# Kernel tuning notes

Measured on AMD Instinct MI355X. Metric: run time of the kernel, lower is better.

Reference implementation:

```python
import jax, jax.numpy as jnp
import numpy as np


def setup_inputs() -> dict:
    key = jax.random.key(0)
    B, D, KD, TR, NI = 4096, 512, 448, 64, 16  # batch, d_model, key_dim_size, t_resolution, num_iters
    DK = KD + TR                                # full query/key width = 512
    ks = jax.random.split(key, 9)

    def w(k, fan_in, fan_out):
        return jax.random.normal(k, (fan_in, fan_out), jnp.float32) / jnp.sqrt(jnp.float32(fan_in))

    return {
        "x":   jax.random.normal(ks[0], (B, D), jnp.float32),
        "Wik": w(ks[1], D, KD),        # input_key_proj
        "Wiv": w(ks[2], D, D),         # input_value_proj (value dim = d_model)
        "Wq":  w(ks[3], D, DK),        # query_proj
        "Wk":  w(ks[4], D + TR, DK),   # key_proj on concat(block_out, sin(t*t_enc))
        "Wv":  w(ks[5], D, D),         # value_proj
        "W1":  w(ks[6], D, D),         # block MLP layer 1
        "W2":  w(ks[7], D, D),         # block MLP layer 2
        "t_emb": 0.02 * jax.random.normal(ks[8], (NI + 1, D), jnp.float32),  # block time conditioning
    }


def reference(x, Wik, Wiv, Wq, Wk, Wv, W1, W2, t_emb):
    B, D = x.shape
    DK = Wq.shape[1]
    TR = Wk.shape[0] - D           # t_resolution
    NI = t_emb.shape[0] - 1        # num_iters
    dt = x.dtype
    scale = jnp.asarray(1.0 / np.sqrt(DK), dt)
    # t_encoding = pi * (1/2)**i
    t_enc = jnp.pi * (0.5 ** jnp.arange(TR, dtype=dt))

    def attend(q, K, V, n):  # q:[B,DK], K:[B,NI,DK], V:[B,NI,D]; n static valid length
        s = jnp.einsum('bd,btd->bt', q, K[:, :n]) * scale
        p = jax.nn.softmax(s, axis=-1)
        return jnp.einsum('bt,btd->bd', p, V[:, :n])

    def block(A, t):  # opaque self.block(A, t=t): MLP with per-t conditioning
        return jax.nn.gelu(A @ W1 + t_emb[t]) @ W2

    # preallocated growing KV cache (in-place append instead of concat)
    K = jnp.zeros((B, NI, DK), dt)
    V = jnp.zeros((B, NI, D), dt)
    k0 = jnp.pad(x @ Wik, ((0, 0), (0, TR)))  # initial key padded to DK (sin(0)=0 encoding)
    K = K.at[:, 0].set(k0)
    V = V.at[:, 0].set(x @ Wiv)
    q = jnp.ones((B, DK), dt)

    for t in range(NI - 1):  # static unrolled recurrence over iterations
        A = attend(q, K, V, t + 1)
        Bt = block(A, t)
        sin_t = jnp.broadcast_to(jnp.sin(t * t_enc), (B, TR))
        K = K.at[:, t + 1].set(jnp.concatenate([Bt, sin_t], axis=-1) @ Wk)
        V = V.at[:, t + 1].set(Bt @ Wv)
        q = Bt @ Wq

    A = attend(q, K, V, NI)
    return block(A, NI)  # final block call with t = num_iters
```

## Files before the change

### kernel.cpp

```cpp
#include <hip/hip_runtime.h>
#include <hip/hip_bf16.h>
#include <math.h>

typedef unsigned short u16;
using bf16x8 = __attribute__((ext_vector_type(8))) short;
using f32x4  = __attribute__((ext_vector_type(4))) float;

__device__ inline float b2f(u16 u) {
  unsigned v = ((unsigned)u) << 16;
  return __builtin_bit_cast(float, v);
}
__device__ inline u16 f2b(float f) {
  unsigned u = __builtin_bit_cast(unsigned, f);
  u += 0x7fffu + ((u >> 16) & 1u);
  return (u16)(u >> 16);
}
__device__ inline float gelu_f(float x) {
  float x3 = x * x * x;
  return 0.5f * x * (1.f + tanhf(0.7978845608028654f * (x + 0.044715f * x3)));
}
__device__ inline void gload_lds16(const void* g, void* lds) {
  __builtin_amdgcn_global_load_lds((const __attribute__((address_space(1))) void*)g,
                                   (__attribute__((address_space(3))) void*)lds,
                                   16, 0, 0);
}

#define EPI_SPLIT2 0
#define EPI_F32    1

template<int EPI>
__global__ __launch_bounds__(256)
void gemm64(const u16* __restrict__ Aptr, int lda,
            const u16* __restrict__ BT,
            void* __restrict__ out0, void* __restrict__ out1,
            const u16* __restrict__ fvec, int t1)
{
  constexpr int BM = 128, BN = 64, WN = 32, NR = 2, MR = 4;
  __shared__ alignas(16) char Ash[2][BM * 128];
  __shared__ alignas(16) char Bsh[2][BN * 128];
  const int tid = threadIdx.x, lane = tid & 63, wid = tid >> 6;
  const int wm = wid >> 1, wn = wid & 1;
  const int bm = blockIdx.x, bn = blockIdx.y;

  const int rIn = lane >> 3;
  const int c16log = (lane & 7) ^ (rIn & 7);

  auto stage = [&](int buf, int kt) {
    #pragma unroll
    for (int i = 0; i < 4; ++i) {
      int c = wid * 4 + i;
      int row = c * 8 + rIn;
      gload_lds16(Aptr + (size_t)(bm * BM + row) * lda + kt + c16log * 8,
                  Ash[buf] + c * 1024);
    }
    #pragma unroll
    for (int i = 0; i < 2; ++i) {
      int c = wid * 2 + i;
      int row = c * 8 + rIn;
      gload_lds16(BT + (size_t)(bn * BN + row) * 512 + kt + c16log * 8,
                  Bsh[buf] + c * 1024);
    }
  };

  f32x4 acc[MR][NR] = {};
  stage(0, 0);
  #pragma unroll
  for (int kt = 0; kt < 8; ++kt) {
    const int c = kt & 1;
    if (kt < 7) stage(c ^ 1, (kt + 1) * 64);
    if (kt < 7) asm volatile("s_waitcnt vmcnt(6)" ::: "memory");
    else        asm volatile("s_waitcnt vmcnt(0)" ::: "memory");
    __builtin_amdgcn_s_barrier();
    asm volatile("" ::: "memory");
    #pragma unroll
    for (int kk = 0; kk < 64; kk += 32) {
      bf16x8 af[MR], bfr[NR];
      #pragma unroll
      for (int m = 0; m < MR; ++m) {
        int R = wm * 64 + m * 16 + (lane & 15);
        int c16 = (kk >> 3) + (lane >> 4);
        af[m] = *(const bf16x8*)(Ash[c] + R * 128 + ((c16 ^ (R & 7)) << 4));
      }
      #pragma unroll
      for (int n = 0; n < NR; ++n) {
        int R = wn * WN + n * 16 + (lane & 15);
        int c16 = (kk >> 3) + (lane >> 4);
        bfr[n] = *(const bf16x8*)(Bsh[c] + R * 128 + ((c16 ^ (R & 7)) << 4));
      }
      #pragma unroll
      for (int m = 0; m < MR; ++m)
        #pragma unroll
        for (int n = 0; n < NR; ++n)
          acc[m][n] = __builtin_amdgcn_mfma_f32_16x16x32_bf16(af[m], bfr[n], acc[m][n], 0, 0, 0);
    }
    asm volatile("" ::: "memory");
    __builtin_amdgcn_s_barrier();
    asm volatile("" ::: "memory");
  }

  const int row0 = bm * BM + wm * 64;
  const int col0 = bn * BN + wn * WN;
  #pragma unroll
  for (int m = 0; m < MR; ++m) {
    #pragma unroll
    for (int n = 0; n < NR; ++n) {
      #pragma unroll
      for (int i = 0; i < 4; ++i) {
        int row = row0 + m * 16 + (lane >> 4) * 4 + i;
        int col = col0 + n * 16 + (lane & 15);
        float v = acc[m][n][i];
        if constexpr (EPI == EPI_SPLIT2) {
          if (col < 512) {
            ((u16*)out0)[((size_t)row * 16 + t1) * 512 + col] = f2b(v + b2f(fvec[col]));
          } else {
            ((u16*)out1)[((size_t)row * 16 + t1) * 512 + (col - 512)] = f2b(v);
          }
        } else {
          ((float*)out0)[(size_t)row * 512 + col] = v;
        }
      }
    }
  }
}

struct BatchJobs {
  const u16* A[5];
  const u16* BT[5];
  u16* O[5];
  int M[5];
};

__global__ __launch_bounds__(256)
void gemm_batch(BatchJobs jb)
{
  constexpr int BM = 128, BN = 64, WN = 32, NR = 2, MR = 4;
  const int z = blockIdx.z;
  if ((int)blockIdx.x * BM >= jb.M[z]) return;
  const u16* __restrict__ Aptr = jb.A[z];
  const u16* __restrict__ BT   = jb.BT[z];
  u16* __restrict__ Optr       = jb.O[z];

  __shared__ alignas(16) char Ash[2][BM * 128];
  __shared__ alignas(16) char Bsh[2][BN * 128];
  const int tid = threadIdx.x, lane = tid & 63, wid = tid >> 6;
  const int wm = wid >> 1, wn = wid & 1;
  const int bm = blockIdx.x, bn = blockIdx.y;

  const int rIn = lane >> 3;
  const int c16log = (lane & 7) ^ (rIn & 7);

  auto stage = [&](int buf, int kt) {
    #pragma unroll
    for (int i = 0; i < 4; ++i) {
      int c = wid * 4 + i;
      int row = c * 8 + rIn;
      gload_lds16(Aptr + (size_t)(bm * BM + row) * 512 + kt + c16log * 8,
                  Ash[buf] + c * 1024);
    }
    #pragma unroll
    for (int i = 0; i < 2; ++i) {
      int c = wid * 2 + i;
      int row = c * 8 + rIn;
      gload_lds16(BT + (size_t)(bn * BN + row) * 512 + kt + c16log * 8,
                  Bsh[buf] + c * 1024);
    }
  };

  f32x4 acc[MR][NR] = {};
  stage(0, 0);
  #pragma unroll
  for (int kt = 0; kt < 8; ++kt) {
    const int c = kt & 1;
    if (kt < 7) stage(c ^ 1, (kt + 1) * 64);
    if (kt < 7) asm volatile("s_waitcnt vmcnt(6)" ::: "memory");
    else        asm volatile("s_waitcnt vmcnt(0)" ::: "memory");
    __builtin_amdgcn_s_barrier();
    asm volatile("" ::: "memory");
    #pragma unroll
    for (int kk = 0; kk < 64; kk += 32) {
      bf16x8 af[MR], bfr[NR];
      #pragma unroll
      for (int m = 0; m < MR; ++m) {
        int R = wm * 64 + m * 16 + (lane & 15);
        int c16 = (kk >> 3) + (lane >> 4);
        af[m] = *(const bf16x8*)(Ash[c] + R * 128 + ((c16 ^ (R & 7)) << 4));
      }
      #pragma unroll
      for (int n = 0; n < NR; ++n) {
        int R = wn * WN + n * 16 + (lane & 15);
        int c16 = (kk >> 3) + (lane >> 4);
        bfr[n] = *(const bf16x8*)(Bsh[c] + R * 128 + ((c16 ^ (R & 7)) << 4));
      }
      #pragma unroll
      for (int m = 0; m < MR; ++m)
        #pragma unroll
        for (int n = 0; n < NR; ++n)
          acc[m][n] = __builtin_amdgcn_mfma_f32_16x16x32_bf16(af[m], bfr[n], acc[m][n], 0, 0, 0);
    }
    asm volatile("" ::: "memory");
    __builtin_amdgcn_s_barrier();
    asm volatile("" ::: "memory");
  }

  const int row0 = bm * BM + wm * 64;
  const int col0 = bn * BN + wn * WN;
  #pragma unroll
  for (int m = 0; m < MR; ++m)
    #pragma unroll
    for (int n = 0; n < NR; ++n)
      #pragma unroll
      for (int i = 0; i < 4; ++i) {
        int row = row0 + m * 16 + (lane >> 4) * 4 + i;
        int col = col0 + n * 16 + (lane & 15);
        Optr[(size_t)row * 512 + col] = f2b(acc[m][n][i]);
      }
}

__global__ __launch_bounds__(256)
void attend_kernel(const u16* __restrict__ qv, const u16* __restrict__ Kc,
                   const u16* __restrict__ VWc, u16* __restrict__ Hout,
                   const float* __restrict__ temb, int n)
{
  const int lane = threadIdx.x & 63;
  const int w = threadIdx.x >> 6;
  const int b = blockIdx.x * 4 + w;
  const float scale = 0.04419417382415922f;
  const size_t base = (size_t)b * 512 + lane * 8;
  bf16x8 q8 = *(const bf16x8*)(qv + base);
  float qf[8];
  #pragma unroll
  for (int j = 0; j < 8; ++j) qf[j] = b2f((u16)q8[j]);
  float s[16];
  float mx = -1e30f;
  #pragma unroll
  for (int t = 0; t < 16; ++t) {
    if (t < n) {
      bf16x8 k8 = *(const bf16x8*)(Kc + ((size_t)b * 16 + t) * 512 + lane * 8);
      float d = 0.f;
      #pragma unroll
      for (int j = 0; j < 8; ++j) d += qf[j] * b2f((u16)k8[j]);
      #pragma unroll
      for (int off = 32; off > 0; off >>= 1) d += __shfl_xor(d, off, 64);
      s[t] = d * scale;
      mx = fmaxf(mx, s[t]);
    }
  }
  float p[16], sum = 0.f;
  #pragma unroll
  for (int t = 0; t < 16; ++t) if (t < n) { p[t] = expf(s[t] - mx); sum += p[t]; }
  const float inv = 1.f / sum;
  float a[8] = {};
  #pragma unroll
  for (int t = 0; t < 16; ++t) {
    if (t < n) {
      bf16x8 v8 = *(const bf16x8*)(VWc + ((size_t)b * 16 + t) * 512 + lane * 8);
      float pt = p[t] * inv;
      #pragma unroll
      for (int j = 0; j < 8; ++j) a[j] += pt * b2f((u16)v8[j]);
    }
  }
  bf16x8 o;
  #pragma unroll
  for (int j = 0; j < 8; ++j)
    o[j] = (short)f2b(gelu_f(a[j] + temb[lane * 8 + j]));
  *(bf16x8*)(Hout + base) = o;
}

__global__ __launch_bounds__(256)
void prep_kernel(const float* __restrict__ x,   const float* __restrict__ Wik,
                 const float* __restrict__ Wiv, const float* __restrict__ Wq,
                 const float* __restrict__ Wk,  const float* __restrict__ Wv,
                 const float* __restrict__ W1,  const float* __restrict__ W2,
                 u16* __restrict__ W1T, u16* __restrict__ W2T, u16* __restrict__ WqT,
                 u16* __restrict__ WkT, u16* __restrict__ WvT,
                 u16* __restrict__ W2b, u16* __restrict__ Wivb, u16* __restrict__ xb,
                 u16* __restrict__ Wikpadb, u16* __restrict__ biasKpad)
{
  const int bid = blockIdx.x, tid = threadIdx.x;
  if (bid < 1280) {
    __shared__ float tile[32][33];
    const int mat = bid >> 8, local = bid & 255;
    const float* in = (mat == 0) ? W1 : (mat == 1) ? W2 : (mat == 2) ? Wq
                    : (mat == 3) ? Wk : Wv;
    u16* out = (mat == 0) ? W1T : (mat == 1) ? W2T : (mat == 2) ? WqT
             : (mat == 3) ? WkT : WvT;
    const int tx = tid & 31, ty = tid >> 5;
    const int c0 = (local & 15) * 32, r0 = (local >> 4) * 32;
    #pragma unroll
    for (int rr = 0; rr < 32; rr += 8)
      tile[ty + rr][tx] = in[(size_t)(r0 + ty + rr) * 512 + c0 + tx];
    __syncthreads();
    #pragma unroll
    for (int rr = 0; rr < 32; rr += 8)
      out[(size_t)(c0 + ty + rr) * 512 + r0 + tx] = f2b(tile[tx][ty + rr]);
  } else if (bid < 3840) {
    const float* in; u16* out; int local;
    if (bid < 1536)      { in = W2;  out = W2b;  local = bid - 1280; }
    else if (bid < 1792) { in = Wiv; out = Wivb; local = bid - 1536; }
    else                 { in = x;   out = xb;   local = bid - 1792; }
    const int i = local * 256 + tid;
    const float4 v = ((const float4*)in)[i];
    ushort4 o;
    o.x = f2b(v.x); o.y = f2b(v.y); o.z = f2b(v.z); o.w = f2b(v.w);
    ((ushort4*)out)[i] = o;
  } else if (bid < 4096) {
    const int local = bid - 3840;
    const int e = local * 1024 + tid * 4;
    const int r = e >> 9, c0 = e & 511;
    ushort4 o;
    float v0 = (c0 + 0 < 448) ? Wik[(size_t)r * 448 + c0 + 0] : 0.f;
    float v1 = (c0 + 1 < 448) ? Wik[(size_t)r * 448 + c0 + 1] : 0.f;
    float v2 = (c0 + 2 < 448) ? Wik[(size_t)r * 448 + c0 + 2] : 0.f;
    float v3 = (c0 + 3 < 448) ? Wik[(size_t)r * 448 + c0 + 3] : 0.f;
    o.x = f2b(v0); o.y = f2b(v1); o.z = f2b(v2); o.w = f2b(v3);
    *(ushort4*)(Wikpadb + (size_t)r * 512 + c0) = o;
  } else {
    const int local = bid - 4096;
    const int t = local >> 1;
    const int col = ((local & 1) << 8) + tid;
    float acc = 0.f;
    if (t < 15) {
      #pragma unroll
      for (int r = 0; r < 64; ++r) {
        float tenc = 3.14159265358979323846f * exp2f(-(float)r);
        acc += sinf((float)t * tenc) * Wk[(size_t)(512 + r) * 512 + col];
      }
    }
    biasKpad[(size_t)t * 512 + col] = f2b(acc);
  }
}

extern "C" void kernel_launch(void* const* d_in, const int* in_sizes, int n_in,
                              void* d_out, int out_size, void* d_ws, size_t ws_size,
                              hipStream_t stream)
{
  const float* x    = (const float*)d_in[0];
  const float* Wik  = (const float*)d_in[1];
  const float* Wiv  = (const float*)d_in[2];
  const float* Wq   = (const float*)d_in[3];
  const float* Wk   = (const float*)d_in[4];
  const float* Wv   = (const float*)d_in[5];
  const float* W1   = (const float*)d_in[6];
  const float* W2   = (const float*)d_in[7];
  const float* temb = (const float*)d_in[8];

  char* ws = (char*)d_ws;
  size_t off = 0;
  auto alloc = [&](size_t bytes) {
    char* p = ws + off;
    off += (bytes + 255) & ~(size_t)255;
    return p;
  };
  const size_t SQ = (size_t)512 * 512 * 2;
  u16* W1T     = (u16*)alloc(SQ);
  u16* W2T     = (u16*)alloc(SQ);
  u16* WqT     = (u16*)alloc(SQ);
  u16* WkT     = (u16*)alloc(SQ);
  u16* WvT     = (u16*)alloc(SQ);
  u16* W2b     = (u16*)alloc(SQ);
  u16* Wivb    = (u16*)alloc(SQ);
  u16* Wikpadb = (u16*)alloc(SQ);
  u16* biasKpad= (u16*)alloc((size_t)128 * 512 * 2);
  u16* W2Wq    = (u16*)alloc(SQ);
  u16* W2WkD   = (u16*)alloc(SQ);
  u16* W2Wv    = (u16*)alloc(SQ);
  u16* biasC   = (u16*)alloc((size_t)128 * 512 * 2);
  u16* PT2     = (u16*)alloc((size_t)1024 * 512 * 2);
  u16* ITn     = (u16*)alloc((size_t)1024 * 512 * 2);
  u16* xb      = (u16*)alloc((size_t)4096 * 512 * 2);
  u16* Kc      = (u16*)alloc((size_t)4096 * 16 * 512 * 2);
  u16* VWc     = (u16*)alloc((size_t)4096 * 16 * 512 * 2);
  u16* Hb      = (u16*)alloc((size_t)4096 * 512 * 2);

  dim3 blk(256);
  prep_kernel<<<dim3(4352), blk, 0, stream>>>(
      x, Wik, Wiv, Wq, Wk, Wv, W1, W2,
      W1T, W2T, WqT, WkT, WvT, W2b, Wivb, xb, Wikpadb, biasKpad);

  BatchJobs b1 = {};
  b1.A[0] = W2b; b1.BT[0] = WqT; b1.O[0] = W2Wq;  b1.M[0] = 512;
  b1.A[1] = W2b; b1.BT[1] = WkT; b1.O[1] = W2WkD; b1.M[1] = 512;
  b1.A[2] = W2b; b1.BT[2] = WvT; b1.O[2] = W2Wv;  b1.M[2] = 512;
  gemm_batch<<<dim3(4, 8, 3), blk, 0, stream>>>(b1);

  BatchJobs b2 = {};
  b2.A[0] = W2Wq;     b2.BT[0] = W2WkD;   b2.O[0] = PT2;                       b2.M[0] = 512;
  b2.A[1] = W1T;      b2.BT[1] = W2Wv;    b2.O[1] = PT2 + (size_t)512 * 512;   b2.M[1] = 512;
  b2.A[2] = W2Wq;     b2.BT[2] = Wikpadb; b2.O[2] = ITn;                       b2.M[2] = 512;
  b2.A[3] = W1T;      b2.BT[3] = Wivb;    b2.O[3] = ITn + (size_t)512 * 512;   b2.M[3] = 512;
  b2.A[4] = biasKpad; b2.BT[4] = W2Wq;    b2.O[4] = biasC;                     b2.M[4] = 128;
  gemm_batch<<<dim3(4, 8, 5), blk, 0, stream>>>(b2);

  gemm64<EPI_SPLIT2><<<dim3(32, 16), blk, 0, stream>>>(
      xb, 512, ITn, Kc, VWc, biasC + (size_t)15 * 512, 0);

  for (int t = 0; t < 15; ++t) {
    attend_kernel<<<dim3(1024), blk, 0, stream>>>(
        Hb, Kc, VWc, Hb, temb + (size_t)t * 512, t + 1);
    gemm64<EPI_SPLIT2><<<dim3(32, 16), blk, 0, stream>>>(
        Hb, 512, PT2, Kc, VWc, biasC + (size_t)t * 512, t + 1);
  }
  attend_kernel<<<dim3(1024), blk, 0, stream>>>(
      Hb, Kc, VWc, Hb, temb + (size_t)16 * 512, 16);
  gemm64<EPI_F32><<<dim3(32, 8), blk, 0, stream>>>(
      Hb, 512, W2T, d_out, nullptr, nullptr, 0);
}
```

Measured before the change: 519.7 us.

## Triple-buffer GEMM K-loop and fold first attend step into initial projection epilogue

The GEMM kernels move from double to triple buffering of their LDS tiles, issuing loads two k-tiles ahead with adjusted waitcnt thresholds so more memory latency is hidden. The initial projection GEMM gets a new epilogue that writes K/V slot 0 and also computes the first hidden state directly as gelu(v + temb[0]). This works because the first attention over a single key is an identity on V, so one attend launch is removed and the loop is reordered. The cost is 50% more LDS per block, which may lower occupancy, plus extra per-element GELU work in the init epilogue.

```diff
diff --git a/kernel.cpp b/kernel.cpp
--- a/kernel.cpp
+++ b/kernel.cpp
@@ -27,17 +27,18 @@
 
 #define EPI_SPLIT2 0
 #define EPI_F32    1
+#define EPI_INIT2H 2
 
 template<int EPI>
 __global__ __launch_bounds__(256)
 void gemm64(const u16* __restrict__ Aptr, int lda,
             const u16* __restrict__ BT,
-            void* __restrict__ out0, void* __restrict__ out1,
-            const u16* __restrict__ fvec, int t1)
+            void* __restrict__ out0, void* __restrict__ out1, void* __restrict__ out2,
+            const u16* __restrict__ fvec, const float* __restrict__ tembv, int t1)
 {
   constexpr int BM = 128, BN = 64, WN = 32, NR = 2, MR = 4;
-  __shared__ alignas(16) char Ash[2][BM * 128];
-  __shared__ alignas(16) char Bsh[2][BN * 128];
+  __shared__ alignas(16) char Ash[3][BM * 128];
+  __shared__ alignas(16) char Bsh[3][BN * 128];
   const int tid = threadIdx.x, lane = tid & 63, wid = tid >> 6;
   const int wm = wid >> 1, wn = wid & 1;
   const int bm = blockIdx.x, bn = blockIdx.y;
@@ -64,12 +65,18 @@
 
   f32x4 acc[MR][NR] = {};
   stage(0, 0);
+  stage(1, 64);
   #pragma unroll
   for (int kt = 0; kt < 8; ++kt) {
-    const int c = kt & 1;
-    if (kt < 7) stage(c ^ 1, (kt + 1) * 64);
-    if (kt < 7) asm volatile("s_waitcnt vmcnt(6)" ::: "memory");
-    else        asm volatile("s_waitcnt vmcnt(0)" ::: "memory");
+    const int cb = kt % 3;
+    if (kt < 6) {
+      stage((kt + 2) % 3, (kt + 2) * 64);
+      asm volatile("s_waitcnt vmcnt(12)" ::: "memory");
+    } else if (kt == 6) {
+      asm volatile("s_waitcnt vmcnt(6)" ::: "memory");
+    } else {
+      asm volatile("s_waitcnt vmcnt(0)" ::: "memory");
+    }
     __builtin_amdgcn_s_barrier();
     asm volatile("" ::: "memory");
     #pragma unroll
@@ -79,13 +86,13 @@
       for (int m = 0; m < MR; ++m) {
         int R = wm * 64 + m * 16 + (lane & 15);
         int c16 = (kk >> 3) + (lane >> 4);
-        af[m] = *(const bf16x8*)(Ash[c] + R * 128 + ((c16 ^ (R & 7)) << 4));
+        af[m] = *(const bf16x8*)(Ash[cb] + R * 128 + ((c16 ^ (R & 7)) << 4));
       }
       #pragma unroll
       for (int n = 0; n < NR; ++n) {
         int R = wn * WN + n * 16 + (lane & 15);
         int c16 = (kk >> 3) + (lane >> 4);
-        bfr[n] = *(const bf16x8*)(Bsh[c] + R * 128 + ((c16 ^ (R & 7)) << 4));
+        bfr[n] = *(const bf16x8*)(Bsh[cb] + R * 128 + ((c16 ^ (R & 7)) << 4));
       }
       #pragma unroll
       for (int m = 0; m < MR; ++m)
@@ -115,6 +122,14 @@
           } else {
             ((u16*)out1)[((size_t)row * 16 + t1) * 512 + (col - 512)] = f2b(v);
           }
+        } else if constexpr (EPI == EPI_INIT2H) {
+          if (col < 512) {
+            ((u16*)out0)[(size_t)row * 16 * 512 + col] = f2b(v);
+          } else {
+            ((u16*)out1)[(size_t)row * 16 * 512 + (col - 512)] = f2b(v);
+            ((u16*)out2)[(size_t)row * 512 + (col - 512)] =
+                f2b(gelu_f(v + tembv[col - 512]));
+          }
         } else {
           ((float*)out0)[(size_t)row * 512 + col] = v;
         }
@@ -140,8 +155,8 @@
   const u16* __restrict__ BT   = jb.BT[z];
   u16* __restrict__ Optr       = jb.O[z];
 
-  __shared__ alignas(16) char Ash[2][BM * 128];
-  __shared__ alignas(16) char Bsh[2][BN * 128];
+  __shared__ alignas(16) char Ash[3][BM * 128];
+  __shared__ alignas(16) char Bsh[3][BN * 128];
   const int tid = threadIdx.x, lane = tid & 63, wid = tid >> 6;
   const int wm = wid >> 1, wn = wid & 1;
   const int bm = blockIdx.x, bn = blockIdx.y;
@@ -168,12 +183,18 @@
 
   f32x4 acc[MR][NR] = {};
   stage(0, 0);
+  stage(1, 64);
   #pragma unroll
   for (int kt = 0; kt < 8; ++kt) {
-    const int c = kt & 1;
-    if (kt < 7) stage(c ^ 1, (kt + 1) * 64);
-    if (kt < 7) asm volatile("s_waitcnt vmcnt(6)" ::: "memory");
-    else        asm volatile("s_waitcnt vmcnt(0)" ::: "memory");
+    const int cb = kt % 3;
+    if (kt < 6) {
+      stage((kt + 2) % 3, (kt + 2) * 64);
+      asm volatile("s_waitcnt vmcnt(12)" ::: "memory");
+    } else if (kt == 6) {
+      asm volatile("s_waitcnt vmcnt(6)" ::: "memory");
+    } else {
+      asm volatile("s_waitcnt vmcnt(0)" ::: "memory");
+    }
     __builtin_amdgcn_s_barrier();
     asm volatile("" ::: "memory");
     #pragma unroll
@@ -183,13 +204,13 @@
       for (int m = 0; m < MR; ++m) {
         int R = wm * 64 + m * 16 + (lane & 15);
         int c16 = (kk >> 3) + (lane >> 4);
-        af[m] = *(const bf16x8*)(Ash[c] + R * 128 + ((c16 ^ (R & 7)) << 4));
+        af[m] = *(const bf16x8*)(Ash[cb] + R * 128 + ((c16 ^ (R & 7)) << 4));
       }
       #pragma unroll
       for (int n = 0; n < NR; ++n) {
         int R = wn * WN + n * 16 + (lane & 15);
         int c16 = (kk >> 3) + (lane >> 4);
-        bfr[n] = *(const bf16x8*)(Bsh[c] + R * 128 + ((c16 ^ (R & 7)) << 4));
+        bfr[n] = *(const bf16x8*)(Bsh[cb] + R * 128 + ((c16 ^ (R & 7)) << 4));
       }
       #pragma unroll
       for (int m = 0; m < MR; ++m)
@@ -391,17 +412,16 @@
   b2.A[4] = biasKpad; b2.BT[4] = W2Wq;    b2.O[4] = biasC;                     b2.M[4] = 128;
   gemm_batch<<<dim3(4, 8, 5), blk, 0, stream>>>(b2);
 
-  gemm64<EPI_SPLIT2><<<dim3(32, 16), blk, 0, stream>>>(
-      xb, 512, ITn, Kc, VWc, biasC + (size_t)15 * 512, 0);
+  gemm64<EPI_INIT2H><<<dim3(32, 16), blk, 0, stream>>>(
+      xb, 512, ITn, Kc, VWc, Hb, nullptr, temb, 0);
 
   for (int t = 0; t < 15; ++t) {
+    gemm64<EPI_SPLIT2><<<dim3(32, 16), blk, 0, stream>>>(
+        Hb, 512, PT2, Kc, VWc, nullptr, biasC + (size_t)t * 512, nullptr, t + 1);
+    const int ti = (t == 14) ? 16 : t + 1;
     attend_kernel<<<dim3(1024), blk, 0, stream>>>(
-        Hb, Kc, VWc, Hb, temb + (size_t)t * 512, t + 1);
-    gemm64<EPI_SPLIT2><<<dim3(32, 16), blk, 0, stream>>>(
-        Hb, 512, PT2, Kc, VWc, biasC + (size_t)t * 512, t + 1);
-  }
-  attend_kernel<<<dim3(1024), blk, 0, stream>>>(
-      Hb, Kc, VWc, Hb, temb + (size_t)16 * 512, 16);
+        Hb, Kc, VWc, Hb, temb + (size_t)ti * 512, t + 2);
+  }
   gemm64<EPI_F32><<<dim3(32, 8), blk, 0, stream>>>(
-      Hb, 512, W2T, d_out, nullptr, nullptr, 0);
-}
+      Hb, 512, W2T, d_out, nullptr, nullptr, nullptr, nullptr, 0);
+}
```

Result: no change. 518.7 us (-0.2%).
